# Kernel tuning notes

Hardware: AMD Instinct MI355X
Metric: run time of the kernel (lower is better)

Reference implementation:

```python
import jax, jax.numpy as jnp
import numpy as np

B, C, H, W = 2, 128, 64, 64
D_STATE = 16
EXPAND = 2
D_INNER = C * EXPAND          # 256
DT_RANK = -(-C // 16)         # 8
K = 4                         # scan directions
COMPRESS = 3
SQUEEZE = 30
EPS = 1e-5


def layernorm(x, g, b):
    mu = x.mean(-1, keepdims=True)
    xm = x - mu
    var = (xm * xm).mean(-1, keepdims=True)
    return xm * jax.lax.rsqrt(var + EPS) * g + b


def conv2d(x, w, bias, pad):
    y = jax.lax.conv_general_dilated(x, w, (1, 1), ((pad, pad), (pad, pad)),
                                     dimension_numbers=('NCHW', 'OIHW', 'NCHW'))
    return y + bias[None, :, None, None]


def selective_scan(xs, dts, A, Bs, Cs):
    # xs,dts: (B,K,D,L); A: (K,D,N); Bs,Cs: (B,K,N,L)
    dt_t = jnp.moveaxis(dts, -1, 0)
    x_t = jnp.moveaxis(xs, -1, 0)
    B_t = jnp.moveaxis(Bs, -1, 0)
    C_t = jnp.moveaxis(Cs, -1, 0)
    h0 = jnp.zeros(xs.shape[:3] + (A.shape[-1],), xs.dtype)

    def step(h, inp):
        dt_l, x_l, b_l, c_l = inp          # (B,K,D),(B,K,D),(B,K,N),(B,K,N)
        dA = jnp.exp(dt_l[..., None] * A)  # (B,K,D,N)
        h = dA * h + (dt_l * x_l)[..., None] * b_l[:, :, None, :]
        y = jnp.einsum('bkdn,bkn->bkd', h, c_l)
        return h, y

    _, ys = jax.lax.scan(step, h0, (dt_t, x_t, B_t, C_t))
    return jnp.moveaxis(ys, 0, -1)  # (B,K,D,L)


def ss2d(x, p):  # x: (B,H,W,C) -> (B,H,W,C)
    xz = x @ p['in_proj_w'].T
    xc, z = jnp.split(xz, 2, axis=-1)
    xc = xc.transpose(0, 3, 1, 2)  # (B,D,H,W)
    xc = jax.lax.conv_general_dilated(xc, p['conv_w'], (1, 1), ((1, 1), (1, 1)),
                                      feature_group_count=D_INNER,
                                      dimension_numbers=('NCHW', 'OIHW', 'NCHW'))
    xc = jax.nn.silu(xc + p['conv_b'][None, :, None, None])
    b, d, h, w = xc.shape
    L = h * w
    x_hw = xc.reshape(b, d, L)
    x_wh = xc.transpose(0, 1, 3, 2).reshape(b, d, L)
    xs = jnp.stack([x_hw, x_wh, x_hw[..., ::-1], x_wh[..., ::-1]], axis=1)  # (B,4,D,L)
    x_dbl = jnp.einsum('bkdl,kcd->bkcl', xs, p['x_proj_w'])
    dtr, Bs, Cs = jnp.split(x_dbl, [DT_RANK, DT_RANK + D_STATE], axis=2)
    dts = jnp.einsum('bkrl,kdr->bkdl', dtr, p['dt_w'])
    dts = jax.nn.softplus(dts + p['dt_b'][None, :, :, None])
    A = -jnp.exp(p['A_logs']).reshape(K, d, D_STATE)
    ys = selective_scan(xs, dts, A, Bs, Cs)
    ys = ys + xs * p['Ds'].reshape(K, d)[None, :, :, None]
    inv = ys[:, 2:4][..., ::-1]  # undo flipped scans
    wh = lambda t: t.reshape(b, d, w, h).transpose(0, 1, 3, 2).reshape(b, d, L)
    y = ys[:, 0] + inv[:, 0] + wh(ys[:, 1]) + wh(inv[:, 1])
    y = y.transpose(0, 2, 1).reshape(b, h, w, d)
    y = layernorm(y, p['out_norm_g'], p['out_norm_b'])
    y = y * jax.nn.silu(z)
    return y @ p['out_proj_w'].T


def cab(x, p):  # x: (B,C,H,W)
    t = jax.nn.gelu(conv2d(x, p['cab_w1'], p['cab_b1'], 1), approximate=False)
    t = conv2d(t, p['cab_w2'], p['cab_b2'], 1)
    s = t.mean((2, 3), keepdims=True)
    s = jax.nn.relu(conv2d(s, p['ca_w1'], p['ca_b1'], 0))
    s = jax.nn.sigmoid(conv2d(s, p['ca_w2'], p['ca_b2'], 0))
    return t * s


def vss_block(input, p):
    inp = input.transpose(0, 2, 3, 1)  # (B,H,W,C)
    x = inp * p['skip_scale'] + ss2d(layernorm(inp, p['ln1_g'], p['ln1_b']), p)
    c = cab(layernorm(x, p['ln2_g'], p['ln2_b']).transpose(0, 3, 1, 2), p)
    x = x * p['skip_scale2'] + c.transpose(0, 2, 3, 1)
    return x.transpose(0, 3, 1, 2)


def setup_inputs() -> dict:
    key = jax.random.key(0)
    ks = jax.random.split(key, 16)
    rn = lambda i, shp, s=0.02: jax.random.normal(ks[i], shp, jnp.float32) * s
    return {
        'input': jax.random.normal(ks[0], (B, C, H, W), jnp.float32),
        'ln1_g': jnp.ones((C,), jnp.float32), 'ln1_b': jnp.zeros((C,), jnp.float32),
        'skip_scale': jnp.ones((C,), jnp.float32), 'skip_scale2': jnp.ones((C,), jnp.float32),
        'ln2_g': jnp.ones((C,), jnp.float32), 'ln2_b': jnp.zeros((C,), jnp.float32),
        'in_proj_w': rn(1, (2 * D_INNER, C)),
        'conv_w': rn(2, (D_INNER, 1, 3, 3), 0.1),
        'conv_b': jnp.zeros((D_INNER,), jnp.float32),
        'x_proj_w': rn(3, (K, DT_RANK + 2 * D_STATE, D_INNER)),
        'dt_w': rn(4, (K, D_INNER, DT_RANK), 0.1),
        'dt_b': rn(5, (K, D_INNER), 0.1),
        'A_logs': jnp.log(jnp.tile(jnp.arange(1, D_STATE + 1, dtype=jnp.float32), (K * D_INNER, 1))),
        'Ds': jnp.ones((K * D_INNER,), jnp.float32),
        'out_norm_g': jnp.ones((D_INNER,), jnp.float32), 'out_norm_b': jnp.zeros((D_INNER,), jnp.float32),
        'out_proj_w': rn(6, (C, D_INNER)),
        'cab_w1': rn(7, (C // COMPRESS, C, 3, 3), 0.05),
        'cab_b1': jnp.zeros((C // COMPRESS,), jnp.float32),
        'cab_w2': rn(8, (C, C // COMPRESS, 3, 3), 0.05),
        'cab_b2': jnp.zeros((C,), jnp.float32),
        'ca_w1': rn(9, (C // SQUEEZE, C, 1, 1), 0.05),
        'ca_b1': jnp.zeros((C // SQUEEZE,), jnp.float32),
        'ca_w2': rn(10, (C, C // SQUEEZE, 1, 1), 0.05),
        'ca_b2': jnp.zeros((C,), jnp.float32),
    }


def reference(input, ln1_g, ln1_b, skip_scale, skip_scale2, ln2_g, ln2_b,
              in_proj_w, conv_w, conv_b, x_proj_w, dt_w, dt_b, A_logs, Ds,
              out_norm_g, out_norm_b, out_proj_w,
              cab_w1, cab_b1, cab_w2, cab_b2, ca_w1, ca_b1, ca_w2, ca_b2):
    p = dict(ln1_g=ln1_g, ln1_b=ln1_b, skip_scale=skip_scale, skip_scale2=skip_scale2,
             ln2_g=ln2_g, ln2_b=ln2_b, in_proj_w=in_proj_w, conv_w=conv_w, conv_b=conv_b,
             x_proj_w=x_proj_w, dt_w=dt_w, dt_b=dt_b, A_logs=A_logs, Ds=Ds,
             out_norm_g=out_norm_g, out_norm_b=out_norm_b, out_proj_w=out_proj_w,
             cab_w1=cab_w1, cab_b1=cab_b1, cab_w2=cab_w2, cab_b2=cab_b2,
             ca_w1=ca_w1, ca_b1=ca_b1, ca_w2=ca_w2, ca_b2=ca_b2)
    return vss_block(input, p)
```

## Files before the change

kernel.cpp:

```cpp
#include <hip/hip_runtime.h>
#include <math.h>

#define BB 2
#define CC 128
#define HH 64
#define WW 64
#define LL 4096
#define DI 256
#define NS 16
#define KK 4
#define OC1 42

#define NC 256
#define CL 16

#define K3_POS 16
#define BCW 48

__device__ __forceinline__ float sigmoidf_(float x) { return 1.f / (1.f + __expf(-x)); }
__device__ __forceinline__ float siluf_(float x)    { return x * sigmoidf_(x); }

__device__ __forceinline__ int scan_pos(int k, int i) {
  if (k == 0) return i;
  if (k == 1) return ((i & 63) << 6) | (i >> 6);
  if (k == 2) return (LL - 1) - i;
  int j = (LL - 1) - i;
  return ((j & 63) << 6) | (j >> 6);
}

__global__ __launch_bounds__(256) void k1_ln_inproj(
    const float* __restrict__ inp, const float* __restrict__ g, const float* __restrict__ b,
    const float* __restrict__ wproj, float* __restrict__ xcin, float* __restrict__ zbuf) {
  __shared__ float sx[64][132];
  __shared__ float sw[128][68];
  __shared__ float smu[64], srs[64];
  const int tid = threadIdx.x;
  const int rt = blockIdx.x & 3;
  const int pt = blockIdx.x >> 2;
  const int bb = pt >> 6;
  const int pbase = (pt & 63) << 6;

  for (int idx = tid; idx < 64 * CC; idx += 256) {
    int c = idx >> 6, pl = idx & 63;
    sx[pl][c] = inp[((size_t)bb * CC + c) * LL + pbase + pl];
  }
  __syncthreads();
  {
    int pl = tid >> 2, j = tid & 3;
    float s = 0.f, s2 = 0.f;
    for (int c = j; c < CC; c += 4) { float v = sx[pl][c]; s += v; s2 += v * v; }
    s += __shfl_xor(s, 1); s2 += __shfl_xor(s2, 1);
    s += __shfl_xor(s, 2); s2 += __shfl_xor(s2, 2);
    if (j == 0) {
      float mu = s * (1.f / CC);
      smu[pl] = mu;
      srs[pl] = rsqrtf(s2 * (1.f / CC) - mu * mu + 1e-5f);
    }
  }
  __syncthreads();
  for (int idx = tid; idx < 64 * CC; idx += 256) {
    int c = idx & 127, pl = idx >> 7;
    sx[pl][c] = (sx[pl][c] - smu[pl]) * srs[pl] * g[c] + b[c];
  }

  const int pg = tid & 7, rg = tid >> 3;
  float acc[8][4];
#pragma unroll
  for (int j = 0; j < 8; j++)
#pragma unroll
    for (int q = 0; q < 4; q++) acc[j][q] = 0.f;

  for (int kc = 0; kc < CC; kc += 64) {
    __syncthreads();
    for (int idx = tid; idx < 128 * 64; idx += 256) {
      int cl = idx & 63, rl = idx >> 6;
      sw[rl][cl] = wproj[(size_t)(rt * 128 + rl) * CC + kc + cl];
    }
    __syncthreads();
#pragma unroll 4
    for (int i = 0; i < 16; i++) {
      const int k0 = kc + 4 * i, kl0 = 4 * i;
      float4 xv[8], wv[4];
#pragma unroll
      for (int j = 0; j < 8; j++) xv[j] = *(const float4*)&sx[pg + 8 * j][k0];
#pragma unroll
      for (int q = 0; q < 4; q++) wv[q] = *(const float4*)&sw[rg + 32 * q][kl0];
#pragma unroll
      for (int j = 0; j < 8; j++)
#pragma unroll
        for (int q = 0; q < 4; q++) {
          acc[j][q] += xv[j].x * wv[q].x + xv[j].y * wv[q].y
                     + xv[j].z * wv[q].z + xv[j].w * wv[q].w;
        }
    }
  }

  float* buf = (rt < 2) ? xcin : zbuf;
  const int drow = (rt & 1) * 128;
#pragma unroll
  for (int j = 0; j < 8; j++) {
    const int p = pbase + pg + 8 * j;
    float* dst = buf + ((size_t)bb * LL + p) * DI + drow;
#pragma unroll
    for (int q = 0; q < 4; q++) dst[rg + 32 * q] = acc[j][q];
  }
}

__global__ __launch_bounds__(256) void k2_dwconv(
    const float* __restrict__ xcin, const float* __restrict__ cw, const float* __restrict__ cb,
    float* __restrict__ xconv) {
  const int w0 = (blockIdx.x & 7) * 8;
  const int hh = (blockIdx.x >> 3) & 63;
  const int bb = blockIdx.x >> 9;
  const int d = threadIdx.x;

  float wv[9];
#pragma unroll
  for (int kk = 0; kk < 9; kk++) wv[kk] = cw[d * 9 + kk];
  const float bias = cb[d];

  float xin[3][10];
#pragma unroll
  for (int kh = 0; kh < 3; kh++) {
    int r = hh + kh - 1;
    bool vr = (r >= 0 && r < HH);
#pragma unroll
    for (int c = 0; c < 10; c++) {
      int cc2 = w0 + c - 1;
      bool vc = (cc2 >= 0 && cc2 < WW);
      xin[kh][c] = (vr && vc) ? xcin[((size_t)bb * LL + r * WW + cc2) * DI + d] : 0.f;
    }
  }
#pragma unroll
  for (int j = 0; j < 8; j++) {
    float acc = bias;
#pragma unroll
    for (int kh = 0; kh < 3; kh++)
#pragma unroll
      for (int kw = 0; kw < 3; kw++)
        acc += wv[kh * 3 + kw] * xin[kh][j + kw];
    xconv[((size_t)bb * LL + hh * WW + w0 + j) * DI + d] = siluf_(acc);
  }
}

__global__ __launch_bounds__(256) void k3_proj(
    const float* __restrict__ xconv, const float* __restrict__ xpw,
    float* __restrict__ BCbuf) {
  __shared__ float sv[K3_POS][260];
  const int tid = threadIdx.x;
  const int bb = blockIdx.x >> 8;
  const int pbase = (blockIdx.x & 255) << 4;

  for (int idx = tid; idx < K3_POS * DI; idx += 256) {
    int d = idx & 255, pl = idx >> 8;
    sv[pl][d] = xconv[((size_t)bb * LL + pbase + pl) * DI + d];
  }
  __syncthreads();

  const int rb = tid >> 4, pg = tid & 15;
  const int r0 = rb * 10;
  float acc[10];
#pragma unroll
  for (int q = 0; q < 10; q++) acc[q] = 0.f;

  const float4* wf = (const float4*)xpw;
#pragma unroll 4
  for (int i = 0; i < DI / 4; i++) {
    float4 xv = *(const float4*)&sv[pg][i * 4];
#pragma unroll
    for (int q = 0; q < 10; q++) {
      float4 wa = wf[(size_t)(r0 + q) * 64 + i];
      acc[q] += wa.x * xv.x + wa.y * xv.y + wa.z * xv.z + wa.w * xv.w;
    }
  }

  const int k = r0 / 40, c0 = r0 - k * 40;
  float* dst = BCbuf + ((size_t)(bb * KK + k) * LL + pbase + pg) * BCW + c0;
#pragma unroll
  for (int q = 0; q < 10; q++) dst[q] = acc[q];
}

__global__ __launch_bounds__(256) void k4a_chunk(
    const float* __restrict__ xconv, const float* __restrict__ BCbuf,
    const float* __restrict__ A_logs, const float* __restrict__ dtw,
    const float* __restrict__ dtb,
    float* __restrict__ csA, float* __restrict__ csB) {
  __shared__ float sBC[CL][26];
  const int d = threadIdx.x;
  const int chunk = blockIdx.x & (NC - 1);
  const int t = blockIdx.x / NC;
  const int k = t & 3;
  const int bb = t >> 2;
  const int bk = bb * KK + k;
  const int base = chunk * CL;

  for (int idx = d; idx < CL * 24; idx += 256) {
    int ii = idx / 24, j = idx - ii * 24;
    int pos = scan_pos(k, base + ii);
    sBC[ii][j] = BCbuf[((size_t)bk * LL + pos) * BCW + j];
  }
  float a[NS];
  bool fast = true;
#pragma unroll
  for (int n = 0; n < NS; n++) {
    a[n] = -__expf(A_logs[((size_t)k * DI + d) * NS + n]);
    fast = fast && (fabsf(a[n] + (float)(n + 1)) < 1e-3f * (n + 1));
  }
  const float* wdt = dtw + ((size_t)k * DI + d) * 8;
  const float4 wd0 = *(const float4*)wdt;
  const float4 wd1 = *(const float4*)(wdt + 4);
  const float bdt = dtb[k * DI + d];
  __syncthreads();

  const float* x_p = xconv + (size_t)bb * LL * DI + d;

  float Ap[NS], Bc[NS];
#pragma unroll
  for (int n = 0; n < NS; n++) { Ap[n] = 1.f; Bc[n] = 0.f; }

  if (fast) {
    float sumdt = 0.f;
#pragma unroll
    for (int half = 0; half < CL / 8; half++) {
      float xvr[8];
#pragma unroll
      for (int j = 0; j < 8; j++)
        xvr[j] = x_p[(size_t)scan_pos(k, base + half * 8 + j) * DI];
#pragma unroll
      for (int j = 0; j < 8; j++) {
        const int ii = half * 8 + j;
        const float* dr = sBC[ii];
        float u = bdt + wd0.x * dr[0] + wd0.y * dr[1] + wd0.z * dr[2] + wd0.w * dr[3]
                      + wd1.x * dr[4] + wd1.y * dr[5] + wd1.z * dr[6] + wd1.w * dr[7];
        float t2 = __expf(u);
        float E = __builtin_amdgcn_rcpf(1.f + t2);
        float dt = u > 20.f ? u : -0.69314718056f * __log2f(E);
        sumdt += dt;
        float dtx = dt * xvr[j];
        float E2 = E * E;
        float dA1 = E, dA2 = E2;
#pragma unroll
        for (int n = 0; n < NS; n += 2) {
          Bc[n] = dA1 * Bc[n] + dtx * sBC[ii][8 + n];
          Bc[n + 1] = dA2 * Bc[n + 1] + dtx * sBC[ii][9 + n];
          dA1 *= E2; dA2 *= E2;
        }
      }
    }
    float Et = __expf(-sumdt);
    float p = Et;
#pragma unroll
    for (int n = 0; n < NS; n++) { Ap[n] = p; p *= Et; }
  } else {
#pragma unroll 2
    for (int ii = 0; ii < CL; ii++) {
      int pos = scan_pos(k, base + ii);
      float xv = x_p[(size_t)pos * DI];
      const float* dr = sBC[ii];
      float u = bdt + wd0.x * dr[0] + wd0.y * dr[1] + wd0.z * dr[2] + wd0.w * dr[3]
                    + wd1.x * dr[4] + wd1.y * dr[5] + wd1.z * dr[6] + wd1.w * dr[7];
      float t2 = __expf(u);
      float dt = u > 20.f ? u : log1pf(t2);
      float dtx = dt * xv;
#pragma unroll
      for (int n = 0; n < NS; n++) {
        float dA = __expf(dt * a[n]);
        Ap[n] *= dA;
        Bc[n] = dA * Bc[n] + dtx * sBC[ii][8 + n];
      }
    }
  }
  size_t e = ((size_t)(bk * NC + chunk) * NS) * DI + d;
#pragma unroll
  for (int n = 0; n < NS; n++) {
    csA[e + (size_t)n * DI] = Ap[n];
    csB[e + (size_t)n * DI] = Bc[n];
  }
}

__global__ __launch_bounds__(256) void k4b_scanchunks(
    float* csAh, const float* __restrict__ csB) {
  const int d = threadIdx.x;
  const int n = blockIdx.x & (NS - 1);
  const int bk = blockIdx.x >> 4;
  const size_t stride = (size_t)NS * DI;
  size_t e = ((size_t)bk * NC * NS + n) * DI + d;
  float H = 0.f;
  for (int c0 = 0; c0 < NC; c0 += 16) {
    float A[16], Bv[16];
#pragma unroll
    for (int j = 0; j < 16; j++) {
      A[j]  = csAh[e + (size_t)j * stride];
      Bv[j] = csB[e + (size_t)j * stride];
    }
#pragma unroll
    for (int j = 0; j < 16; j++) {
      csAh[e + (size_t)j * stride] = H;
      H = A[j] * H + Bv[j];
    }
    e += (size_t)16 * stride;
  }
}

__global__ __launch_bounds__(256) void k4c_scan(
    const float* __restrict__ xconv, const float* __restrict__ BCbuf,
    const float* __restrict__ A_logs, const float* __restrict__ dtw,
    const float* __restrict__ dtb, const float* __restrict__ Ds,
    const float* __restrict__ hin, float* __restrict__ ys) {
  __shared__ float sBC[CL][BCW];
  const int d = threadIdx.x;
  const int chunk = blockIdx.x & (NC - 1);
  const int t = blockIdx.x / NC;
  const int k = t & 3;
  const int bb = t >> 2;
  const int bk = bb * KK + k;
  const int base = chunk * CL;

  for (int idx = d; idx < CL * 40; idx += 256) {
    int ii = idx / 40, j = idx - ii * 40;
    int pos = scan_pos(k, base + ii);
    sBC[ii][j] = BCbuf[((size_t)bk * LL + pos) * BCW + j];
  }
  float a[NS], h[NS];
  bool fast = true;
  const size_t eh = ((size_t)(bk * NC + chunk) * NS) * DI + d;
#pragma unroll
  for (int n = 0; n < NS; n++) {
    a[n] = -__expf(A_logs[((size_t)k * DI + d) * NS + n]);
    fast = fast && (fabsf(a[n] + (float)(n + 1)) < 1e-3f * (n + 1));
    h[n] = hin[eh + (size_t)n * DI];
  }
  const float* wdt = dtw + ((size_t)k * DI + d) * 8;
  const float4 wd0 = *(const float4*)wdt;
  const float4 wd1 = *(const float4*)(wdt + 4);
  const float bdt = dtb[k * DI + d];
  const float Dd = Ds[k * DI + d];
  __syncthreads();

  const float* x_p = xconv + (size_t)bb * LL * DI + d;
  float* ys_p = ys + (size_t)bk * LL * DI + d;

  if (fast) {
#pragma unroll
    for (int half = 0; half < CL / 8; half++) {
      float xvr[8];
#pragma unroll
      for (int j = 0; j < 8; j++)
        xvr[j] = x_p[(size_t)scan_pos(k, base + half * 8 + j) * DI];
#pragma unroll
      for (int j = 0; j < 8; j++) {
        const int ii = half * 8 + j;
        const float* dr = sBC[ii];
        float u = bdt + wd0.x * dr[0] + wd0.y * dr[1] + wd0.z * dr[2] + wd0.w * dr[3]
                      + wd1.x * dr[4] + wd1.y * dr[5] + wd1.z * dr[6] + wd1.w * dr[7];
        float t2 = __expf(u);
        float E = __builtin_amdgcn_rcpf(1.f + t2);
        float dt = u > 20.f ? u : -0.69314718056f * __log2f(E);
        float dtx = dt * xvr[j];
        float y = xvr[j] * Dd;
        float E2 = E * E;
        float dA1 = E, dA2 = E2;
#pragma unroll
        for (int n = 0; n < NS; n += 2) {
          h[n] = dA1 * h[n] + dtx * sBC[ii][8 + n];
          y += h[n] * sBC[ii][24 + n];
          h[n + 1] = dA2 * h[n + 1] + dtx * sBC[ii][9 + n];
          y += h[n + 1] * sBC[ii][25 + n];
          dA1 *= E2; dA2 *= E2;
        }
        ys_p[(size_t)scan_pos(k, base + ii) * DI] = y;
      }
    }
  } else {
#pragma unroll 2
    for (int ii = 0; ii < CL; ii++) {
      int pos = scan_pos(k, base + ii);
      float xv = x_p[(size_t)pos * DI];
      const float* dr = sBC[ii];
      float u = bdt + wd0.x * dr[0] + wd0.y * dr[1] + wd0.z * dr[2] + wd0.w * dr[3]
                    + wd1.x * dr[4] + wd1.y * dr[5] + wd1.z * dr[6] + wd1.w * dr[7];
      float t2 = __expf(u);
      float dt = u > 20.f ? u : log1pf(t2);
      float dtx = dt * xv;
      float y = xv * Dd;
#pragma unroll
      for (int n = 0; n < NS; n++) {
        float dA = __expf(dt * a[n]);
        h[n] = dA * h[n] + dtx * sBC[ii][8 + n];
        y += h[n] * sBC[ii][24 + n];
      }
      ys_p[(size_t)pos * DI] = y;
    }
  }
}

__global__ __launch_bounds__(256) void k5_combine(
    const float* __restrict__ ys, const float* __restrict__ zbuf,
    const float* __restrict__ ong, const float* __restrict__ onb,
    const float* __restrict__ opw, const float* __restrict__ inp,
    const float* __restrict__ sk, const float* __restrict__ g2, const float* __restrict__ b2,
    float* __restrict__ xres, float* __restrict__ ln2) {
  __shared__ float sy[8][260];
  __shared__ float sr[8][132];
  __shared__ float smu[8], srs[8];
  const int tid = threadIdx.x;
  const int bb = blockIdx.x >> 9;
  const int pbase = (blockIdx.x & 511) << 3;

  for (int idx = tid; idx < 8 * DI; idx += 256) {
    int d = idx & 255, pl = idx >> 8;
    size_t o0 = (((size_t)bb * KK + 0) * LL + pbase + pl) * DI + d;
    const size_t st = (size_t)LL * DI;
    sy[pl][d] = ys[o0] + ys[o0 + st] + ys[o0 + 2 * st] + ys[o0 + 3 * st];
  }
  __syncthreads();
  {
    int pl = tid >> 5, j = tid & 31;
    float s = 0.f, s2 = 0.f;
    for (int d = j; d < DI; d += 32) { float v = sy[pl][d]; s += v; s2 += v * v; }
#pragma unroll
    for (int m = 1; m < 32; m <<= 1) { s += __shfl_xor(s, m); s2 += __shfl_xor(s2, m); }
    if (j == 0) {
      float mu = s * (1.f / DI);
      smu[pl] = mu;
      srs[pl] = rsqrtf(s2 * (1.f / DI) - mu * mu + 1e-5f);
    }
  }
  __syncthreads();
  for (int idx = tid; idx < 8 * DI; idx += 256) {
    int d = idx & 255, pl = idx >> 8;
    float zv = zbuf[((size_t)bb * LL + pbase + pl) * DI + d];
    sy[pl][d] = ((sy[pl][d] - smu[pl]) * srs[pl] * ong[d] + onb[d]) * siluf_(zv);
  }
  __syncthreads();
  {
    const int rb = tid >> 3, pg = tid & 7;
    const int c0 = rb * 4;
    float acc[4] = {0.f, 0.f, 0.f, 0.f};
    const float4* wf = (const float4*)opw;
#pragma unroll 4
    for (int i = 0; i < DI / 4; i++) {
      float4 xv = *(const float4*)&sy[pg][i * 4];
#pragma unroll
      for (int q = 0; q < 4; q++) {
        float4 wa = wf[(size_t)(c0 + q) * 64 + i];
        acc[q] += wa.x * xv.x + wa.y * xv.y + wa.z * xv.z + wa.w * xv.w;
      }
    }
    const int p = pbase + pg;
    float r[4];
#pragma unroll
    for (int q = 0; q < 4; q++) {
      r[q] = inp[((size_t)bb * CC + c0 + q) * LL + p] * sk[c0 + q] + acc[q];
      sr[pg][c0 + q] = r[q];
    }
    *(float4*)&xres[((size_t)bb * LL + p) * CC + c0] = make_float4(r[0], r[1], r[2], r[3]);
  }
  __syncthreads();
  {
    int pl = tid >> 5, j = tid & 31;
    float s = 0.f, s2 = 0.f;
    for (int c = j; c < CC; c += 32) { float v = sr[pl][c]; s += v; s2 += v * v; }
#pragma unroll
    for (int m = 1; m < 32; m <<= 1) { s += __shfl_xor(s, m); s2 += __shfl_xor(s2, m); }
    if (j == 0) {
      float mu = s * (1.f / CC);
      smu[pl] = mu;
      srs[pl] = rsqrtf(s2 * (1.f / CC) - mu * mu + 1e-5f);
    }
  }
  __syncthreads();
  for (int idx = tid; idx < 8 * CC; idx += 256) {
    int pl = idx & 7, c = idx >> 3;
    ln2[((size_t)bb * CC + c) * LL + pbase + pl] =
        (sr[pl][c] - smu[pl]) * srs[pl] * g2[c] + b2[c];
  }
}

__global__ __launch_bounds__(256) void k6a_conv1(
    const float* __restrict__ ln2, const float* __restrict__ w1,
    float* __restrict__ pc1) {
  __shared__ float sIn[16][6][68];
  __shared__ float sw[16 * 9 * OC1];
  const int tid = threadIdx.x;
  const int icq = blockIdx.x & 7;
  const int h4  = (blockIdx.x >> 3) & 15;
  const int bb  = blockIdx.x >> 7;
  const int icb = icq * 16;

  for (int idx = tid; idx < 16 * 6 * 66; idx += 256) {
    int i = idx / 396, rem = idx % 396;
    int rr = rem / 66, j = rem % 66;
    int r = h4 * 4 + rr - 1, c2 = j - 1;
    float v = 0.f;
    if (r >= 0 && r < HH && c2 >= 0 && c2 < WW)
      v = ln2[((size_t)bb * CC + icb + i) * LL + r * WW + c2];
    sIn[i][rr][j] = v;
  }
  for (int idx = tid; idx < OC1 * 16 * 9; idx += 256) {
    int oc = idx / 144, rem = idx % 144;
    int i = rem / 9, kk = rem % 9;
    sw[(i * 9 + kk) * OC1 + oc] = w1[((size_t)oc * CC + icb + i) * 9 + kk];
  }
  __syncthreads();

  const int wq = tid & 7, hq = (tid >> 3) & 3, ocg = tid >> 5;
  float acc[6][8];
#pragma unroll
  for (int q = 0; q < 6; q++)
#pragma unroll
    for (int ww = 0; ww < 8; ww++) acc[q][ww] = 0.f;

  for (int i = 0; i < 16; i++) {
    float xin[3][10];
#pragma unroll
    for (int kh = 0; kh < 3; kh++)
#pragma unroll
      for (int j = 0; j < 10; j++) xin[kh][j] = sIn[i][hq + kh][wq * 8 + j];
#pragma unroll
    for (int q = 0; q < 6; q++) {
      int oc = ocg + 8 * q;
      if (oc >= OC1) break;
      float wv[9];
#pragma unroll
      for (int kk = 0; kk < 9; kk++) wv[kk] = sw[(i * 9 + kk) * OC1 + oc];
#pragma unroll
      for (int kh = 0; kh < 3; kh++)
#pragma unroll
        for (int kw = 0; kw < 3; kw++)
#pragma unroll
          for (int ww = 0; ww < 8; ww++)
            acc[q][ww] += wv[kh * 3 + kw] * xin[kh][ww + kw];
    }
  }

  const int hrow = h4 * 4 + hq;
#pragma unroll
  for (int q = 0; q < 6; q++) {
    int oc = ocg + 8 * q;
    if (oc >= OC1) break;
    float* dst = pc1 + (((size_t)icq * BB + bb) * OC1 + oc) * LL + hrow * WW + wq * 8;
    *(float4*)dst       = make_float4(acc[q][0], acc[q][1], acc[q][2], acc[q][3]);
    *(float4*)(dst + 4) = make_float4(acc[q][4], acc[q][5], acc[q][6], acc[q][7]);
  }
}

__global__ __launch_bounds__(256) void k6b_reduce(
    const float* __restrict__ pc1, const float* __restrict__ b1,
    float* __restrict__ t1) {
  const int oc = blockIdx.x % OC1;
  const int bb = blockIdx.x / OC1;
  const float bias = b1[oc];
  const size_t st = (size_t)BB * OC1 * LL;
  const float* src = pc1 + ((size_t)bb * OC1 + oc) * LL;
  float* dst = t1 + ((size_t)bb * OC1 + oc) * LL;
  for (int i = threadIdx.x; i < LL / 4; i += 256) {
    float4 s = ((const float4*)src)[i];
#pragma unroll
    for (int icq = 1; icq < 8; icq++) {
      float4 v = *(const float4*)(src + (size_t)icq * st + i * 4);
      s.x += v.x; s.y += v.y; s.z += v.z; s.w += v.w;
    }
    float r[4] = {s.x + bias, s.y + bias, s.z + bias, s.w + bias};
#pragma unroll
    for (int q = 0; q < 4; q++)
      r[q] = 0.5f * r[q] * (1.f + erff(r[q] * 0.70710678118654752f));
    ((float4*)dst)[i] = make_float4(r[0], r[1], r[2], r[3]);
  }
}

__global__ __launch_bounds__(256) void k7_conv2(
    const float* __restrict__ t1, const float* __restrict__ w2, const float* __restrict__ b2,
    float* __restrict__ t2) {
  __shared__ float sIn[21][4][68];
  __shared__ float sw[21 * 9 * 32];
  const int tid = threadIdx.x;
  const int ocq = blockIdx.x & 3;
  const int h2  = (blockIdx.x >> 2) & 31;
  const int bb  = blockIdx.x >> 7;

  const int wq = tid & 7, hq = (tid >> 3) & 1, ocg = tid >> 4;
  float acc[2][8];
#pragma unroll
  for (int q = 0; q < 2; q++)
#pragma unroll
    for (int ww = 0; ww < 8; ww++) acc[q][ww] = 0.f;

  for (int ch = 0; ch < 2; ch++) {
    const int icb = ch * 21;
    __syncthreads();
    for (int idx = tid; idx < 21 * 4 * 66; idx += 256) {
      int i = idx / 264, rem = idx % 264;
      int rr = rem / 66, j = rem % 66;
      int r = h2 * 2 + rr - 1, c2 = j - 1;
      float v = 0.f;
      if (r >= 0 && r < HH && c2 >= 0 && c2 < WW)
        v = t1[((size_t)bb * OC1 + icb + i) * LL + r * WW + c2];
      sIn[i][rr][j] = v;
    }
    for (int idx = tid; idx < 32 * 21 * 9; idx += 256) {
      int ol = idx / 189, rem = idx % 189;
      int i = rem / 9, kk = rem % 9;
      sw[(i * 9 + kk) * 32 + ol] = w2[((size_t)(ocq * 32 + ol) * OC1 + icb + i) * 9 + kk];
    }
    __syncthreads();

    for (int i = 0; i < 21; i++) {
      float xin[3][10];
#pragma unroll
      for (int kh = 0; kh < 3; kh++)
#pragma unroll
        for (int j = 0; j < 10; j++) xin[kh][j] = sIn[i][hq + kh][wq * 8 + j];
#pragma unroll
      for (int q = 0; q < 2; q++) {
        int ol = ocg + 16 * q;
        float wv[9];
#pragma unroll
        for (int kk = 0; kk < 9; kk++) wv[kk] = sw[(i * 9 + kk) * 32 + ol];
#pragma unroll
        for (int kh = 0; kh < 3; kh++)
#pragma unroll
          for (int kw = 0; kw < 3; kw++)
#pragma unroll
            for (int ww = 0; ww < 8; ww++)
              acc[q][ww] += wv[kh * 3 + kw] * xin[kh][ww + kw];
      }
    }
  }

  const int hrow = h2 * 2 + hq;
#pragma unroll
  for (int q = 0; q < 2; q++) {
    int oc = ocq * 32 + ocg + 16 * q;
    float bias = b2[oc];
    float* dst = t2 + ((size_t)bb * CC + oc) * LL + hrow * WW + wq * 8;
    *(float4*)dst       = make_float4(acc[q][0] + bias, acc[q][1] + bias,
                                      acc[q][2] + bias, acc[q][3] + bias);
    *(float4*)(dst + 4) = make_float4(acc[q][4] + bias, acc[q][5] + bias,
                                      acc[q][6] + bias, acc[q][7] + bias);
  }
}

__global__ __launch_bounds__(256) void k8_mean(const float* __restrict__ t2,
                                               float* __restrict__ smean) {
  __shared__ float red[4];
  const int bc = blockIdx.x;
  const float* src = t2 + (size_t)bc * LL;
  float s = 0.f;
  for (int i = threadIdx.x; i < LL; i += 256) s += src[i];
#pragma unroll
  for (int m = 1; m < 64; m <<= 1) s += __shfl_xor(s, m);
  if ((threadIdx.x & 63) == 0) red[threadIdx.x >> 6] = s;
  __syncthreads();
  if (threadIdx.x == 0) smean[bc] = (red[0] + red[1] + red[2] + red[3]) * (1.f / LL);
}

__global__ __launch_bounds__(256) void k10_final(
    const float* __restrict__ xres, const float* __restrict__ t2,
    const float* __restrict__ smean,
    const float* __restrict__ cw1, const float* __restrict__ cb1,
    const float* __restrict__ cw2, const float* __restrict__ cb2,
    const float* __restrict__ sk2, float* __restrict__ out) {
  __shared__ float mid[4];
  const int tid = threadIdx.x;
  const int bc = blockIdx.x;
  const int bb = bc >> 7, c = bc & 127;

  {
    const int wv = tid >> 6, ln = tid & 63;
    float s = cw1[wv * CC + ln] * smean[bb * CC + ln]
            + cw1[wv * CC + 64 + ln] * smean[bb * CC + 64 + ln];
#pragma unroll
    for (int m = 1; m < 64; m <<= 1) s += __shfl_xor(s, m);
    if (ln == 0) mid[wv] = fmaxf(s + cb1[wv], 0.f);
  }
  __syncthreads();
  float a = cb2[c];
#pragma unroll
  for (int m = 0; m < 4; m++) a += cw2[c * 4 + m] * mid[m];
  const float sv = sigmoidf_(a);

  const float ss = sk2[c];
  const float* t2r = t2 + (size_t)bc * LL;
  float* outr = out + (size_t)bc * LL;
  for (int i = tid; i < LL; i += 256)
    outr[i] = xres[((size_t)bb * LL + i) * CC + c] * ss + t2r[i] * sv;
}


extern "C" void kernel_launch(void* const* d_in, const int* in_sizes, int n_in,
                              void* d_out, int out_size, void* d_ws, size_t ws_size,
                              hipStream_t stream) {
  const float* input      = (const float*)d_in[0];
  const float* ln1_g      = (const float*)d_in[1];
  const float* ln1_b      = (const float*)d_in[2];
  const float* skip_scale = (const float*)d_in[3];
  const float* skip_scale2= (const float*)d_in[4];
  const float* ln2_g      = (const float*)d_in[5];
  const float* ln2_b      = (const float*)d_in[6];
  const float* in_proj_w  = (const float*)d_in[7];
  const float* conv_w     = (const float*)d_in[8];
  const float* conv_b     = (const float*)d_in[9];
  const float* x_proj_w   = (const float*)d_in[10];
  const float* dt_w       = (const float*)d_in[11];
  const float* dt_b       = (const float*)d_in[12];
  const float* A_logs     = (const float*)d_in[13];
  const float* Ds         = (const float*)d_in[14];
  const float* out_norm_g = (const float*)d_in[15];
  const float* out_norm_b = (const float*)d_in[16];
  const float* out_proj_w = (const float*)d_in[17];
  const float* cab_w1     = (const float*)d_in[18];
  const float* cab_b1     = (const float*)d_in[19];
  const float* cab_w2     = (const float*)d_in[20];
  const float* cab_b2     = (const float*)d_in[21];
  const float* ca_w1      = (const float*)d_in[22];
  const float* ca_b1      = (const float*)d_in[23];
  const float* ca_w2      = (const float*)d_in[24];
  const float* ca_b2      = (const float*)d_in[25];

  float* ws = (float*)d_ws;
  float* xcin  = ws;
  float* zbuf  = xcin + (size_t)BB * LL * DI;
  float* xconv = zbuf + (size_t)BB * LL * DI;
  float* BCbuf = xconv + (size_t)BB * LL * DI;
  float* ysb   = BCbuf + (size_t)BB * KK * LL * BCW;
  float* xres  = ysb + (size_t)BB * KK * LL * DI;
  float* ln2b  = xres + (size_t)BB * LL * CC;
  float* t1b   = ln2b + (size_t)BB * CC * LL;
  float* t2b   = t1b + (size_t)BB * OC1 * LL;
  float* smean = t2b + (size_t)BB * CC * LL;
  float* csA   = smean + BB * CC;
  float* csB   = ysb;
  float* pc1   = ysb;

  k1_ln_inproj<<<512, 256, 0, stream>>>(input, ln1_g, ln1_b, in_proj_w, xcin, zbuf);
  k2_dwconv<<<BB * HH * (WW / 8), 256, 0, stream>>>(xcin, conv_w, conv_b, xconv);
  k3_proj<<<BB * (LL / K3_POS), 256, 0, stream>>>(xconv, x_proj_w, BCbuf);
  k4a_chunk<<<BB * KK * NC, 256, 0, stream>>>(xconv, BCbuf, A_logs, dt_w, dt_b, csA, csB);
  k4b_scanchunks<<<BB * KK * NS, 256, 0, stream>>>(csA, csB);
  k4c_scan<<<BB * KK * NC, 256, 0, stream>>>(xconv, BCbuf, A_logs, dt_w, dt_b, Ds, csA, ysb);
  k5_combine<<<BB * (LL / 8), 256, 0, stream>>>(ysb, zbuf, out_norm_g, out_norm_b, out_proj_w,
                                                input, skip_scale, ln2_g, ln2_b, xres, ln2b);
  k6a_conv1<<<BB * 16 * 8, 256, 0, stream>>>(ln2b, cab_w1, pc1);
  k6b_reduce<<<BB * OC1, 256, 0, stream>>>(pc1, cab_b1, t1b);
  k7_conv2<<<BB * 32 * 4, 256, 0, stream>>>(t1b, cab_w2, cab_b2, t2b);
  k8_mean<<<BB * CC, 256, 0, stream>>>(t2b, smean);
  k10_final<<<BB * CC, 256, 0, stream>>>(xres, t2b, smean, ca_w1, ca_b1, ca_w2, ca_b2,
                                         skip_scale2, (float*)d_out);
}
```

Before: 285.0 us.

## Split combine kernel into activation pass and LDS-tiled output projection

The fused combine kernel is split in two. The first kernel sums the four scan directions, applies out_norm and the SiLU gate, and writes the activation to a scratch buffer. The second kernel computes the out_proj GEMM on 16 positions per block, staging 64-wide K-chunks of activations and weights in shared memory so each weight element is reused across more positions. The aim is to cut the repeated per-block global and L2 weight reads of the old kernel, at the cost of an extra global write and read of the activation tensor and one more launch.

```diff
diff --git a/kernel.cpp b/kernel.cpp
--- a/kernel.cpp
+++ b/kernel.cpp
@@ -394,14 +394,11 @@
   }
 }
 
-__global__ __launch_bounds__(256) void k5_combine(
+__global__ __launch_bounds__(256) void k5a_act(
     const float* __restrict__ ys, const float* __restrict__ zbuf,
     const float* __restrict__ ong, const float* __restrict__ onb,
-    const float* __restrict__ opw, const float* __restrict__ inp,
-    const float* __restrict__ sk, const float* __restrict__ g2, const float* __restrict__ b2,
-    float* __restrict__ xres, float* __restrict__ ln2) {
+    float* __restrict__ yact) {
   __shared__ float sy[8][260];
-  __shared__ float sr[8][132];
   __shared__ float smu[8], srs[8];
   const int tid = threadIdx.x;
   const int bb = blockIdx.x >> 9;
@@ -430,48 +427,86 @@
   for (int idx = tid; idx < 8 * DI; idx += 256) {
     int d = idx & 255, pl = idx >> 8;
     float zv = zbuf[((size_t)bb * LL + pbase + pl) * DI + d];
-    sy[pl][d] = ((sy[pl][d] - smu[pl]) * srs[pl] * ong[d] + onb[d]) * siluf_(zv);
+    yact[((size_t)bb * LL + pbase + pl) * DI + d] =
+        ((sy[pl][d] - smu[pl]) * srs[pl] * ong[d] + onb[d]) * siluf_(zv);
+  }
+}
+
+__global__ __launch_bounds__(256) void k5b_proj(
+    const float* __restrict__ yact, const float* __restrict__ opw,
+    const float* __restrict__ inp, const float* __restrict__ sk,
+    const float* __restrict__ g2, const float* __restrict__ b2,
+    float* __restrict__ xres, float* __restrict__ ln2) {
+  __shared__ float sx[16][68];
+  __shared__ float sw[128][68];
+  __shared__ float sr[16][132];
+  __shared__ float smu[16], srs[16];
+  const int tid = threadIdx.x;
+  const int bb = blockIdx.x >> 8;
+  const int pbase = (blockIdx.x & 255) << 4;
+
+  const int pg = tid & 7, rb = tid >> 3;
+  float acc[2][4];
+#pragma unroll
+  for (int j = 0; j < 2; j++)
+#pragma unroll
+    for (int q = 0; q < 4; q++) acc[j][q] = 0.f;
+
+  for (int kc = 0; kc < DI; kc += 64) {
+    __syncthreads();
+    for (int idx = tid; idx < 16 * 64; idx += 256) {
+      int cl = idx & 63, pl = idx >> 6;
+      sx[pl][cl] = yact[((size_t)bb * LL + pbase + pl) * DI + kc + cl];
+    }
+    for (int idx = tid; idx < 128 * 64; idx += 256) {
+      int cl = idx & 63, rl = idx >> 6;
+      sw[rl][cl] = opw[(size_t)rl * DI + kc + cl];
+    }
+    __syncthreads();
+#pragma unroll 4
+    for (int i = 0; i < 16; i++) {
+      float4 xv[2], wv[4];
+#pragma unroll
+      for (int j = 0; j < 2; j++) xv[j] = *(const float4*)&sx[2 * pg + j][4 * i];
+#pragma unroll
+      for (int q = 0; q < 4; q++) wv[q] = *(const float4*)&sw[rb + 32 * q][4 * i];
+#pragma unroll
+      for (int j = 0; j < 2; j++)
+#pragma unroll
+        for (int q = 0; q < 4; q++) {
+          acc[j][q] += xv[j].x * wv[q].x + xv[j].y * wv[q].y
+                     + xv[j].z * wv[q].z + xv[j].w * wv[q].w;
+        }
+    }
+  }
+
+#pragma unroll
+  for (int j = 0; j < 2; j++) {
+    const int p = pbase + 2 * pg + j;
+#pragma unroll
+    for (int q = 0; q < 4; q++) {
+      const int c = rb + 32 * q;
+      float r = inp[((size_t)bb * CC + c) * LL + p] * sk[c] + acc[j][q];
+      xres[((size_t)bb * LL + p) * CC + c] = r;
+      sr[2 * pg + j][c] = r;
+    }
   }
   __syncthreads();
   {
-    const int rb = tid >> 3, pg = tid & 7;
-    const int c0 = rb * 4;
-    float acc[4] = {0.f, 0.f, 0.f, 0.f};
-    const float4* wf = (const float4*)opw;
-#pragma unroll 4
-    for (int i = 0; i < DI / 4; i++) {
-      float4 xv = *(const float4*)&sy[pg][i * 4];
-#pragma unroll
-      for (int q = 0; q < 4; q++) {
-        float4 wa = wf[(size_t)(c0 + q) * 64 + i];
-        acc[q] += wa.x * xv.x + wa.y * xv.y + wa.z * xv.z + wa.w * xv.w;
-      }
-    }
-    const int p = pbase + pg;
-    float r[4];
-#pragma unroll
-    for (int q = 0; q < 4; q++) {
-      r[q] = inp[((size_t)bb * CC + c0 + q) * LL + p] * sk[c0 + q] + acc[q];
-      sr[pg][c0 + q] = r[q];
-    }
-    *(float4*)&xres[((size_t)bb * LL + p) * CC + c0] = make_float4(r[0], r[1], r[2], r[3]);
-  }
-  __syncthreads();
-  {
-    int pl = tid >> 5, j = tid & 31;
+    int pl = tid >> 4, jj = tid & 15;
     float s = 0.f, s2 = 0.f;
-    for (int c = j; c < CC; c += 32) { float v = sr[pl][c]; s += v; s2 += v * v; }
-#pragma unroll
-    for (int m = 1; m < 32; m <<= 1) { s += __shfl_xor(s, m); s2 += __shfl_xor(s2, m); }
-    if (j == 0) {
+    for (int c = jj; c < CC; c += 16) { float v = sr[pl][c]; s += v; s2 += v * v; }
+#pragma unroll
+    for (int m = 1; m < 16; m <<= 1) { s += __shfl_xor(s, m); s2 += __shfl_xor(s2, m); }
+    if (jj == 0) {
       float mu = s * (1.f / CC);
       smu[pl] = mu;
       srs[pl] = rsqrtf(s2 * (1.f / CC) - mu * mu + 1e-5f);
     }
   }
   __syncthreads();
-  for (int idx = tid; idx < 8 * CC; idx += 256) {
-    int pl = idx & 7, c = idx >> 3;
+  for (int idx = tid; idx < 16 * CC; idx += 256) {
+    int pl = idx & 15, c = idx >> 4;
     ln2[((size_t)bb * CC + c) * LL + pbase + pl] =
         (sr[pl][c] - smu[pl]) * srs[pl] * g2[c] + b2[c];
   }
@@ -732,6 +767,7 @@
   float* csA   = smean + BB * CC;
   float* csB   = ysb;
   float* pc1   = ysb;
+  float* yact  = csA;
 
   k1_ln_inproj<<<512, 256, 0, stream>>>(input, ln1_g, ln1_b, in_proj_w, xcin, zbuf);
   k2_dwconv<<<BB * HH * (WW / 8), 256, 0, stream>>>(xcin, conv_w, conv_b, xconv);
@@ -739,8 +775,9 @@
   k4a_chunk<<<BB * KK * NC, 256, 0, stream>>>(xconv, BCbuf, A_logs, dt_w, dt_b, csA, csB);
   k4b_scanchunks<<<BB * KK * NS, 256, 0, stream>>>(csA, csB);
   k4c_scan<<<BB * KK * NC, 256, 0, stream>>>(xconv, BCbuf, A_logs, dt_w, dt_b, Ds, csA, ysb);
-  k5_combine<<<BB * (LL / 8), 256, 0, stream>>>(ysb, zbuf, out_norm_g, out_norm_b, out_proj_w,
-                                                input, skip_scale, ln2_g, ln2_b, xres, ln2b);
+  k5a_act<<<BB * (LL / 8), 256, 0, stream>>>(ysb, zbuf, out_norm_g, out_norm_b, yact);
+  k5b_proj<<<BB * (LL / 16), 256, 0, stream>>>(yact, out_proj_w, input, skip_scale,
+                                               ln2_g, ln2_b, xres, ln2b);
   k6a_conv1<<<BB * 16 * 8, 256, 0, stream>>>(ln2b, cab_w1, pc1);
   k6b_reduce<<<BB * OC1, 256, 0, stream>>>(pc1, cab_b1, t1b);
   k7_conv2<<<BB * 32 * 4, 256, 0, stream>>>(t1b, cab_w2, cab_b2, t2b);
```

Result: faster. 274.5 us (-3.7%).
